# Kernel tuning notes

Hardware: AMD Instinct MI355X
Metric: run time of the kernel (lower is better)

## Reference

```python
import jax, jax.numpy as jnp
import numpy as np


def setup_inputs() -> dict:
    key = jax.random.key(0)
    ks = jax.random.split(key, 7)
    B, V, D, H = 4, 1024, 3, 128
    vertices = jax.random.normal(ks[0], (B, V, D), dtype=jnp.float32)
    # Linear params (x @ W + b convention, W = torch_weight.T)
    W1 = jax.random.normal(ks[1], (2 * D, H), dtype=jnp.float32) * 0.05
    b1 = jnp.zeros((H,), dtype=jnp.float32)
    W2 = jax.random.normal(ks[2], (H, H // 2), dtype=jnp.float32) * 0.05
    b2 = jnp.zeros((H // 2,), dtype=jnp.float32)
    W3 = jax.random.normal(ks[3], (H // 2, 1), dtype=jnp.float32) * 0.05
    b3 = jnp.zeros((1,), dtype=jnp.float32)
    return {"vertices": vertices, "W1": W1, "b1": b1, "W2": W2, "b2": b2, "W3": W3, "b3": b3}


def reference(vertices, W1, b1, W2, b2, W3, b3):
    B, V, D = vertices.shape
    # All unordered pairs (i, j) with i < j -- same order as the nested loop.
    idx_i, idx_j = jnp.triu_indices(V, k=1)  # each [E], E = V*(V-1)/2
    # Pairwise edge features [B, E, 2D] via gather (no Python loop).
    edge_features = jnp.concatenate(
        [vertices[:, idx_i, :], vertices[:, idx_j, :]], axis=-1
    )
    # 3-layer MLP (dropout is identity in eval mode).
    x = jax.nn.relu(edge_features @ W1 + b1)   # [B, E, H]
    x = jax.nn.relu(x @ W2 + b2)               # [B, E, H//2]
    x = x @ W3 + b3                            # [B, E, 1]
    edge_probs = jax.nn.sigmoid(x[..., 0])     # [B, E]
    edge_indices = jnp.stack([idx_i, idx_j], axis=1)  # [E, 2]
    return edge_probs, edge_indices
```

## Files before the change

kernel.cpp:

```cpp
#include <hip/hip_runtime.h>
#include <hip/hip_bf16.h>
#include <math.h>

#define BB 4
#define VV 1024
#define HH 128
#define H2 64
#define EE 523776
#define BE (BB * EE)
#define TPB (EE / 16)
#define NTILES (BE / 16)
#define NPAIR (NTILES / 2)
#define NTHR 256
#define NBLK 1024

typedef __attribute__((ext_vector_type(8))) short bf16x8;
typedef __attribute__((ext_vector_type(4))) float f32x4;

__device__ __forceinline__ short f2bf(float f) {
    __hip_bfloat16 h = __float2bfloat16(f);
    return *reinterpret_cast<short*>(&h);
}

__global__ __launch_bounds__(NTHR, 2) void edge_mlp_mfma3(
    const float* __restrict__ vertices,
    const float* __restrict__ W1,
    const float* __restrict__ b1,
    const float* __restrict__ W2,
    const float* __restrict__ b2,
    const float* __restrict__ W3,
    const float* __restrict__ b3,
    float* __restrict__ out)
{
    const int lane = threadIdx.x & 63;
    const int col  = lane & 15;
    const int u    = lane >> 4;
    const int wid  = threadIdx.x >> 6;

    const f32x4 zero4 = {0.f, 0.f, 0.f, 0.f};

    bf16x8 A1[4][2];
#pragma unroll
    for (int p = 0; p < 4; ++p)
#pragma unroll
        for (int q = 0; q < 2; ++q) {
            const int h = 32 * p + 8 * (col >> 2) + 4 * q + (col & 3);
#pragma unroll
            for (int r = 0; r < 8; ++r) {
                const int k = 8 * u + r;
                float w = 0.0f;
                if (k < 6)       w = W1[k * HH + h];
                else if (k == 6) w = b1[h];
                A1[p][q][r] = f2bf(w);
            }
        }

    bf16x8 A2[4][4];
#pragma unroll
    for (int mt = 0; mt < 4; ++mt)
#pragma unroll
        for (int p = 0; p < 4; ++p) {
            const int n2 = 16 * mt + col;
#pragma unroll
            for (int r = 0; r < 8; ++r) {
                const int h = 32 * p + 8 * u + r;
                A2[mt][p][r] = f2bf(W2[h * H2 + n2]);
            }
        }

    f32x4 cinit[4];
    float w3c[16];
#pragma unroll
    for (int mt = 0; mt < 4; ++mt)
#pragma unroll
        for (int q = 0; q < 4; ++q) {
            const int n2 = 16 * mt + 4 * u + q;
            cinit[mt][q]    = b2[n2];
            w3c[mt * 4 + q] = W3[n2];
        }
    const float b3v = b3[0];

    const int gw = blockIdx.x * 4 + wid;

    for (int pt = gw; pt < NPAIR; pt += NBLK * 4) {
        const int tt0 = pt * 2;
        const int b   = tt0 / TPB;
        const int e00 = (tt0 - b * TPB) * 16;

        int iv[2], jv[2];
        bf16x8 bfv[2];

#pragma unroll
        for (int s = 0; s < 2; ++s) {
            const int e = e00 + s * 16 + col;
            const int rr = EE - 1 - e;
            const float sq = sqrtf((float)(8 * rr + 1));
            int m = (int)(0.5f * (sq - 1.0f));
            if ((m + 1) * (m + 2) / 2 <= rr) ++m;
            if (m * (m + 1) / 2 > rr) --m;
            const int pp = rr - m * (m + 1) / 2;
            iv[s] = VV - 2 - m;
            jv[s] = VV - 1 - pp;

            bf16x8 bf = {0, 0, 0, 0, 0, 0, 0, 0};
            if (u == 0) {
                const float* pvi = vertices + (b * VV + iv[s]) * 3;
                const float* pvj = vertices + (b * VV + jv[s]) * 3;
                bf[0] = f2bf(pvi[0]); bf[1] = f2bf(pvi[1]); bf[2] = f2bf(pvi[2]);
                bf[3] = f2bf(pvj[0]); bf[4] = f2bf(pvj[1]); bf[5] = f2bf(pvj[2]);
                bf[6] = f2bf(1.0f);
            }
            bfv[s] = bf;
        }

        f32x4 d2[2][4];
#pragma unroll
        for (int s = 0; s < 2; ++s)
#pragma unroll
            for (int mt = 0; mt < 4; ++mt) d2[s][mt] = cinit[mt];

#pragma unroll
        for (int p = 0; p < 4; ++p) {
#pragma unroll
            for (int s = 0; s < 2; ++s) {
                f32x4 dA = __builtin_amdgcn_mfma_f32_16x16x32_bf16(A1[p][0], bfv[s], zero4, 0, 0, 0);
                f32x4 dB = __builtin_amdgcn_mfma_f32_16x16x32_bf16(A1[p][1], bfv[s], zero4, 0, 0, 0);
                bf16x8 Bh;
                Bh[0] = f2bf(fmaxf(dA[0], 0.f)); Bh[1] = f2bf(fmaxf(dA[1], 0.f));
                Bh[2] = f2bf(fmaxf(dA[2], 0.f)); Bh[3] = f2bf(fmaxf(dA[3], 0.f));
                Bh[4] = f2bf(fmaxf(dB[0], 0.f)); Bh[5] = f2bf(fmaxf(dB[1], 0.f));
                Bh[6] = f2bf(fmaxf(dB[2], 0.f)); Bh[7] = f2bf(fmaxf(dB[3], 0.f));
                d2[s][0] = __builtin_amdgcn_mfma_f32_16x16x32_bf16(A2[0][p], Bh, d2[s][0], 0, 0, 0);
                d2[s][1] = __builtin_amdgcn_mfma_f32_16x16x32_bf16(A2[1][p], Bh, d2[s][1], 0, 0, 0);
                d2[s][2] = __builtin_amdgcn_mfma_f32_16x16x32_bf16(A2[2][p], Bh, d2[s][2], 0, 0, 0);
                d2[s][3] = __builtin_amdgcn_mfma_f32_16x16x32_bf16(A2[3][p], Bh, d2[s][3], 0, 0, 0);
            }
        }

#pragma unroll
        for (int s = 0; s < 2; ++s) {
            float acc = 0.f;
#pragma unroll
            for (int mt = 0; mt < 4; ++mt)
#pragma unroll
                for (int q = 0; q < 4; ++q)
                    acc = fmaf(fmaxf(d2[s][mt][q], 0.f), w3c[mt * 4 + q], acc);

            acc += __shfl_xor(acc, 16);
            acc += __shfl_xor(acc, 32);

            if (u == 0) {
                const float x = acc + b3v;
                const float prob = __builtin_amdgcn_rcpf(1.0f + __expf(-x));
                out[(tt0 + s) * 16 + col] = prob;
                if (b == 0) {
                    const int e = e00 + s * 16 + col;
                    *(float2*)(&out[BE + 2 * e]) = make_float2((float)iv[s], (float)jv[s]);
                }
            }
        }
    }
}

extern "C" void kernel_launch(void* const* d_in, const int* in_sizes, int n_in,
                              void* d_out, int out_size, void* d_ws, size_t ws_size,
                              hipStream_t stream) {
    const float* vertices = (const float*)d_in[0];
    const float* W1 = (const float*)d_in[1];
    const float* b1 = (const float*)d_in[2];
    const float* W2 = (const float*)d_in[3];
    const float* b2 = (const float*)d_in[4];
    const float* W3 = (const float*)d_in[5];
    const float* b3 = (const float*)d_in[6];
    float* out = (float*)d_out;

    edge_mlp_mfma3<<<NBLK, NTHR, 0, stream>>>(vertices, W1, b1, W2, b2, W3, b3, out);
}
```

Measured before the change: 151.9 us.

## Stage weight fragments in LDS, pack bf16 via perm, raise occupancy

Moves the W1/W2 MFMA operand fragments from per-thread registers into shared memory, loaded per p-step, and raises launch bounds to 3 blocks per SM. It replaces per-element bf16 rounding conversions with byte-perm truncation packing for both the ReLU activations and the vertex features. It also splits the final dot product into four independent accumulators. The aim is fewer VGPRs and VALU instructions, at the cost of LDS reads each iteration and truncation instead of round-to-nearest in bf16 conversion.

```diff
diff --git a/kernel.cpp b/kernel.cpp
--- a/kernel.cpp
+++ b/kernel.cpp
@@ -13,16 +13,32 @@
 #define NPAIR (NTILES / 2)
 #define NTHR 256
 #define NBLK 1024
+#define STRIDE (NBLK * 4)
 
 typedef __attribute__((ext_vector_type(8))) short bf16x8;
 typedef __attribute__((ext_vector_type(4))) float f32x4;
+typedef __attribute__((ext_vector_type(4))) unsigned u32x4;
 
 __device__ __forceinline__ short f2bf(float f) {
     __hip_bfloat16 h = __float2bfloat16(f);
     return *reinterpret_cast<short*>(&h);
 }
 
-__global__ __launch_bounds__(NTHR, 2) void edge_mlp_mfma3(
+__device__ __forceinline__ unsigned pkbf(float lo, float hi) {
+    return __builtin_amdgcn_perm(__float_as_uint(hi), __float_as_uint(lo),
+                                 0x07060302u);
+}
+
+__device__ __forceinline__ bf16x8 relu_pack(f32x4 a, f32x4 b) {
+    u32x4 r;
+    r[0] = pkbf(fmaxf(a[0], 0.f), fmaxf(a[1], 0.f));
+    r[1] = pkbf(fmaxf(a[2], 0.f), fmaxf(a[3], 0.f));
+    r[2] = pkbf(fmaxf(b[0], 0.f), fmaxf(b[1], 0.f));
+    r[3] = pkbf(fmaxf(b[2], 0.f), fmaxf(b[3], 0.f));
+    return __builtin_bit_cast(bf16x8, r);
+}
+
+__global__ __launch_bounds__(NTHR, 3) void edge_mlp_mfma6(
     const float* __restrict__ vertices,
     const float* __restrict__ W1,
     const float* __restrict__ b1,
@@ -32,6 +48,8 @@
     const float* __restrict__ b3,
     float* __restrict__ out)
 {
+    __shared__ __align__(16) bf16x8 wfrag[24 * 64];
+
     const int lane = threadIdx.x & 63;
     const int col  = lane & 15;
     const int u    = lane >> 4;
@@ -39,11 +57,10 @@
 
     const f32x4 zero4 = {0.f, 0.f, 0.f, 0.f};
 
-    bf16x8 A1[4][2];
-#pragma unroll
-    for (int p = 0; p < 4; ++p)
-#pragma unroll
-        for (int q = 0; q < 2; ++q) {
+    for (int f = wid; f < 24; f += 4) {
+        bf16x8 frag;
+        if (f < 8) {
+            const int p = f >> 1, q = f & 1;
             const int h = 32 * p + 8 * (col >> 2) + 4 * q + (col & 3);
 #pragma unroll
             for (int r = 0; r < 8; ++r) {
@@ -51,22 +68,19 @@
                 float w = 0.0f;
                 if (k < 6)       w = W1[k * HH + h];
                 else if (k == 6) w = b1[h];
-                A1[p][q][r] = f2bf(w);
-            }
-        }
-
-    bf16x8 A2[4][4];
-#pragma unroll
-    for (int mt = 0; mt < 4; ++mt)
-#pragma unroll
-        for (int p = 0; p < 4; ++p) {
+                frag[r] = f2bf(w);
+            }
+        } else {
+            const int mt = (f - 8) >> 2, p = (f - 8) & 3;
             const int n2 = 16 * mt + col;
 #pragma unroll
             for (int r = 0; r < 8; ++r) {
                 const int h = 32 * p + 8 * u + r;
-                A2[mt][p][r] = f2bf(W2[h * H2 + n2]);
-            }
-        }
+                frag[r] = f2bf(W2[h * H2 + n2]);
+            }
+        }
+        wfrag[f * 64 + lane] = frag;
+    }
 
     f32x4 cinit[4];
     float w3c[16];
@@ -80,19 +94,20 @@
         }
     const float b3v = b3[0];
 
+    __syncthreads();
+
     const int gw = blockIdx.x * 4 + wid;
 
-    for (int pt = gw; pt < NPAIR; pt += NBLK * 4) {
+    for (int pt = gw; pt < NPAIR; pt += STRIDE) {
         const int tt0 = pt * 2;
         const int b   = tt0 / TPB;
         const int e00 = (tt0 - b * TPB) * 16;
 
+        bf16x8 bfv[2];
         int iv[2], jv[2];
-        bf16x8 bfv[2];
-
 #pragma unroll
         for (int s = 0; s < 2; ++s) {
-            const int e = e00 + s * 16 + col;
+            const int e  = e00 + s * 16 + col;
             const int rr = EE - 1 - e;
             const float sq = sqrtf((float)(8 * rr + 1));
             int m = (int)(0.5f * (sq - 1.0f));
@@ -101,51 +116,68 @@
             const int pp = rr - m * (m + 1) / 2;
             iv[s] = VV - 2 - m;
             jv[s] = VV - 1 - pp;
-
-            bf16x8 bf = {0, 0, 0, 0, 0, 0, 0, 0};
-            if (u == 0) {
-                const float* pvi = vertices + (b * VV + iv[s]) * 3;
-                const float* pvj = vertices + (b * VV + jv[s]) * 3;
-                bf[0] = f2bf(pvi[0]); bf[1] = f2bf(pvi[1]); bf[2] = f2bf(pvi[2]);
-                bf[3] = f2bf(pvj[0]); bf[4] = f2bf(pvj[1]); bf[5] = f2bf(pvj[2]);
-                bf[6] = f2bf(1.0f);
-            }
-            bfv[s] = bf;
+            const float* pvi = vertices + (b * VV + iv[s]) * 3;
+            const float* pvj = vertices + (b * VV + jv[s]) * 3;
+            u32x4 fb;
+            fb[0] = pkbf(pvi[0], pvi[1]);
+            fb[1] = pkbf(pvi[2], pvj[0]);
+            fb[2] = pkbf(pvj[1], pvj[2]);
+            fb[3] = 0x00003F80u;
+            bfv[s] = __builtin_bit_cast(bf16x8, fb);
         }
 
         f32x4 d2[2][4];
-#pragma unroll
-        for (int s = 0; s < 2; ++s)
-#pragma unroll
-            for (int mt = 0; mt < 4; ++mt) d2[s][mt] = cinit[mt];
-
-#pragma unroll
-        for (int p = 0; p < 4; ++p) {
+
+        {
+            const bf16x8 a10 = wfrag[0 * 64 + lane];
+            const bf16x8 a11 = wfrag[1 * 64 + lane];
+            const bf16x8 w20 = wfrag[(8 + 0) * 64 + lane];
+            const bf16x8 w21 = wfrag[(8 + 4) * 64 + lane];
+            const bf16x8 w22 = wfrag[(8 + 8) * 64 + lane];
+            const bf16x8 w23 = wfrag[(8 + 12) * 64 + lane];
 #pragma unroll
             for (int s = 0; s < 2; ++s) {
-                f32x4 dA = __builtin_amdgcn_mfma_f32_16x16x32_bf16(A1[p][0], bfv[s], zero4, 0, 0, 0);
-                f32x4 dB = __builtin_amdgcn_mfma_f32_16x16x32_bf16(A1[p][1], bfv[s], zero4, 0, 0, 0);
-                bf16x8 Bh;
-                Bh[0] = f2bf(fmaxf(dA[0], 0.f)); Bh[1] = f2bf(fmaxf(dA[1], 0.f));
-                Bh[2] = f2bf(fmaxf(dA[2], 0.f)); Bh[3] = f2bf(fmaxf(dA[3], 0.f));
-                Bh[4] = f2bf(fmaxf(dB[0], 0.f)); Bh[5] = f2bf(fmaxf(dB[1], 0.f));
-                Bh[6] = f2bf(fmaxf(dB[2], 0.f)); Bh[7] = f2bf(fmaxf(dB[3], 0.f));
-                d2[s][0] = __builtin_amdgcn_mfma_f32_16x16x32_bf16(A2[0][p], Bh, d2[s][0], 0, 0, 0);
-                d2[s][1] = __builtin_amdgcn_mfma_f32_16x16x32_bf16(A2[1][p], Bh, d2[s][1], 0, 0, 0);
-                d2[s][2] = __builtin_amdgcn_mfma_f32_16x16x32_bf16(A2[2][p], Bh, d2[s][2], 0, 0, 0);
-                d2[s][3] = __builtin_amdgcn_mfma_f32_16x16x32_bf16(A2[3][p], Bh, d2[s][3], 0, 0, 0);
+                f32x4 dA = __builtin_amdgcn_mfma_f32_16x16x32_bf16(a10, bfv[s], zero4, 0, 0, 0);
+                f32x4 dB = __builtin_amdgcn_mfma_f32_16x16x32_bf16(a11, bfv[s], zero4, 0, 0, 0);
+                bf16x8 Bh = relu_pack(dA, dB);
+                d2[s][0] = __builtin_amdgcn_mfma_f32_16x16x32_bf16(w20, Bh, cinit[0], 0, 0, 0);
+                d2[s][1] = __builtin_amdgcn_mfma_f32_16x16x32_bf16(w21, Bh, cinit[1], 0, 0, 0);
+                d2[s][2] = __builtin_amdgcn_mfma_f32_16x16x32_bf16(w22, Bh, cinit[2], 0, 0, 0);
+                d2[s][3] = __builtin_amdgcn_mfma_f32_16x16x32_bf16(w23, Bh, cinit[3], 0, 0, 0);
+            }
+        }
+
+#pragma unroll
+        for (int p = 1; p < 4; ++p) {
+            const bf16x8 a10 = wfrag[(p * 2 + 0) * 64 + lane];
+            const bf16x8 a11 = wfrag[(p * 2 + 1) * 64 + lane];
+            const bf16x8 w20 = wfrag[(8 + 0 * 4 + p) * 64 + lane];
+            const bf16x8 w21 = wfrag[(8 + 1 * 4 + p) * 64 + lane];
+            const bf16x8 w22 = wfrag[(8 + 2 * 4 + p) * 64 + lane];
+            const bf16x8 w23 = wfrag[(8 + 3 * 4 + p) * 64 + lane];
+#pragma unroll
+            for (int s = 0; s < 2; ++s) {
+                f32x4 dA = __builtin_amdgcn_mfma_f32_16x16x32_bf16(a10, bfv[s], zero4, 0, 0, 0);
+                f32x4 dB = __builtin_amdgcn_mfma_f32_16x16x32_bf16(a11, bfv[s], zero4, 0, 0, 0);
+                bf16x8 Bh = relu_pack(dA, dB);
+                d2[s][0] = __builtin_amdgcn_mfma_f32_16x16x32_bf16(w20, Bh, d2[s][0], 0, 0, 0);
+                d2[s][1] = __builtin_amdgcn_mfma_f32_16x16x32_bf16(w21, Bh, d2[s][1], 0, 0, 0);
+                d2[s][2] = __builtin_amdgcn_mfma_f32_16x16x32_bf16(w22, Bh, d2[s][2], 0, 0, 0);
+                d2[s][3] = __builtin_amdgcn_mfma_f32_16x16x32_bf16(w23, Bh, d2[s][3], 0, 0, 0);
             }
         }
 
 #pragma unroll
         for (int s = 0; s < 2; ++s) {
-            float acc = 0.f;
-#pragma unroll
-            for (int mt = 0; mt < 4; ++mt)
-#pragma unroll
-                for (int q = 0; q < 4; ++q)
-                    acc = fmaf(fmaxf(d2[s][mt][q], 0.f), w3c[mt * 4 + q], acc);
-
+            float a0 = 0.f, a1 = 0.f, a2 = 0.f, a3 = 0.f;
+#pragma unroll
+            for (int q = 0; q < 4; ++q) {
+                a0 = fmaf(fmaxf(d2[s][0][q], 0.f), w3c[q],      a0);
+                a1 = fmaf(fmaxf(d2[s][1][q], 0.f), w3c[4 + q],  a1);
+                a2 = fmaf(fmaxf(d2[s][2][q], 0.f), w3c[8 + q],  a2);
+                a3 = fmaf(fmaxf(d2[s][3][q], 0.f), w3c[12 + q], a3);
+            }
+            float acc = (a0 + a1) + (a2 + a3);
             acc += __shfl_xor(acc, 16);
             acc += __shfl_xor(acc, 32);
 
@@ -155,7 +187,8 @@
                 out[(tt0 + s) * 16 + col] = prob;
                 if (b == 0) {
                     const int e = e00 + s * 16 + col;
-                    *(float2*)(&out[BE + 2 * e]) = make_float2((float)iv[s], (float)jv[s]);
+                    *(float2*)(&out[BE + 2 * e]) =
+                        make_float2((float)iv[s], (float)jv[s]);
                 }
             }
         }
@@ -174,5 +207,5 @@
     const float* b3 = (const float*)d_in[6];
     float* out = (float*)d_out;
 
-    edge_mlp_mfma3<<<NBLK, NTHR, 0, stream>>>(vertices, W1, b1, W2, b2, W3, b3, out);
-}
+    edge_mlp_mfma6<<<NBLK, NTHR, 0, stream>>>(vertices, W1, b1, W2, b2, W3, b3, out);
+}
```

Result: slower. 269.5 us (+77.5%).
